# Kernel tuning notes

Hardware: AMD Instinct MI355X
Metric: run time of the kernel (lower is better)

The kernel has to match this reference:

```python
import jax, jax.numpy as jnp
import numpy as np

DIM, NH, NS = 384, 8, 3
HID = int(DIM * 4.0)
R1 = max(1, int(min(DIM, HID) * 0.5))   # 192
R2 = max(1, int(min(HID, DIM) * 0.5))   # 192
SPLIT = DIM // NS                        # 128
HD = DIM // NH                           # 48


def _ln(x, g, b, eps=1e-6):
    m = jnp.mean(x, axis=-1, keepdims=True)
    v = jnp.mean(jnp.square(x - m), axis=-1, keepdims=True)
    return (x - m) * jax.lax.rsqrt(v + eps) * g + b


def _dwconv(x, w, b):
    # x: [B, SPLIT, H, W]; w: [SPLIT, 1, 3, 3] depthwise (groups=SPLIT)
    y = jax.lax.conv_general_dilated(
        x, w, window_strides=(1, 1), padding='SAME',
        dimension_numbers=('NCHW', 'OIHW', 'NCHW'),
        feature_group_count=SPLIT)
    return y + b[None, :, None, None]


def setup_inputs() -> dict:
    key = jax.random.key(0)
    ks = jax.random.split(key, 16)
    s = lambda *sh: 0.02
    inp = {
        'x': jax.random.normal(ks[0], (16, DIM, 56, 56), jnp.float32),
        'dw_w0': jax.random.normal(ks[1], (SPLIT, 1, 3, 3), jnp.float32) * 0.1,
        'dw_b0': jnp.zeros((SPLIT,), jnp.float32),
        'dw_w1': jax.random.normal(ks[2], (SPLIT, 1, 3, 3), jnp.float32) * 0.1,
        'dw_b1': jnp.zeros((SPLIT,), jnp.float32),
        'ln1_g': jnp.ones((DIM,), jnp.float32),
        'ln1_b': jnp.zeros((DIM,), jnp.float32),
        'qkv_w': jax.random.normal(ks[3], (DIM, 3 * DIM), jnp.float32) * 0.02,
        'proj_w': jax.random.normal(ks[4], (DIM, DIM), jnp.float32) * 0.02,
        'proj_b': jnp.zeros((DIM,), jnp.float32),
        'ln2_g': jnp.ones((DIM,), jnp.float32),
        'ln2_b': jnp.zeros((DIM,), jnp.float32),
        'mlp1_dw': jax.random.normal(ks[5], (DIM, R1), jnp.float32) * 0.02,
        'mlp1_uw': jax.random.normal(ks[6], (R1, HID), jnp.float32) * 0.02,
        'mlp1_ub': jnp.zeros((HID,), jnp.float32),
        'mlp2_dw': jax.random.normal(ks[7], (HID, R2), jnp.float32) * 0.02,
        'mlp2_uw': jax.random.normal(ks[8], (R2, DIM), jnp.float32) * 0.02,
        'mlp2_ub': jnp.zeros((DIM,), jnp.float32),
    }
    return inp


def reference(x, dw_w0, dw_b0, dw_w1, dw_b1, ln1_g, ln1_b, qkv_w,
              proj_w, proj_b, ln2_g, ln2_b,
              mlp1_dw, mlp1_uw, mlp1_ub, mlp2_dw, mlp2_uw, mlp2_ub):
    B, C, H, W = x.shape
    # multi-scale depthwise residual chain
    s0, s1, s2 = jnp.split(x, NS, axis=1)
    s1 = _dwconv(s1 + s0, dw_w0, dw_b0)
    s2 = _dwconv(s2 + s1, dw_w1, dw_b1)
    x = jnp.concatenate([s0, s1, s2], axis=1)

    N = H * W
    x_flat = jnp.transpose(x.reshape(B, C, N), (0, 2, 1))  # [B, N, C]
    y = _ln(x_flat, ln1_g, ln1_b)
    qkv = (y @ qkv_w).reshape(B, N, 3, NH, HD)
    q = jnp.transpose(qkv[:, :, 0], (0, 2, 3, 1))  # [B, NH, HD, N]
    k = jnp.transpose(qkv[:, :, 1], (0, 2, 3, 1))
    v = jnp.transpose(qkv[:, :, 2], (0, 2, 3, 1))
    # L2 normalize over token dim (XCA)
    q = q / jnp.maximum(jnp.linalg.norm(q, axis=-1, keepdims=True), 1e-12)
    k = k / jnp.maximum(jnp.linalg.norm(k, axis=-1, keepdims=True), 1e-12)
    attn = jnp.einsum('bhdn,bhen->bhde', q, k)  # [B, NH, HD, HD]
    attn = jax.nn.softmax(attn, axis=-1)
    y = jnp.einsum('bhde,bhen->bhdn', attn, v)  # [B, NH, HD, N]
    y = jnp.transpose(y, (0, 3, 1, 2)).reshape(B, N, C)
    y = y @ proj_w + proj_b
    x_flat = x_flat + y

    z = _ln(x_flat, ln2_g, ln2_b)
    h = jax.nn.gelu((z @ mlp1_dw) @ mlp1_uw + mlp1_ub, approximate=False)
    z = (h @ mlp2_dw) @ mlp2_uw + mlp2_ub
    x_flat = x_flat + z
    return jnp.transpose(x_flat, (0, 2, 1)).reshape(B, C, H, W)
```

## Files before the change

### kernel.cpp

```cpp
#include <hip/hip_runtime.h>


typedef __attribute__((ext_vector_type(8))) short short8;
typedef __attribute__((ext_vector_type(4))) float floatx4;

#define NB 16
#define DIM 384
#define NTOK 3136
#define TTOK 50176
#define NH 8
#define HD 48

__device__ __forceinline__ unsigned short f2bf(float f) {
  union { float f; unsigned int u; } v; v.f = f;
  unsigned int u = v.u;
  unsigned int r = (u + 0x7FFFu + ((u >> 16) & 1u)) >> 16;
  return (unsigned short)r;
}
__device__ __forceinline__ float bf2f(unsigned short h) {
  union { unsigned int u; float f; } v; v.u = ((unsigned int)h) << 16;
  return v.f;
}

__device__ __forceinline__ void gload_lds16(const unsigned short* g, unsigned short* l) {
  __builtin_amdgcn_global_load_lds(
      (const __attribute__((address_space(1))) unsigned int*)g,
      (__attribute__((address_space(3))) unsigned int*)l, 16, 0, 0);
}

__global__ void wtrans(const float* __restrict__ w, unsigned short* __restrict__ wt,
                       int K, int N) {
  int g = blockIdx.x * 256 + threadIdx.x;
  if (g < K * N) {
    int k = g / N, n = g % N;
    wt[(size_t)n * K + k] = f2bf(w[g]);
  }
}

__global__ void dwconv(const float* __restrict__ a, long bsA,
                       const float* __restrict__ b2, long bsB,
                       const float* __restrict__ w, const float* __restrict__ bias,
                       float* __restrict__ dst) {
  int g = blockIdx.x * 256 + threadIdx.x;
  int xx = g % 56;
  int yy = (g / 56) % 56;
  int c  = (g / NTOK) % 128;
  int b  = g / (NTOK * 128);
  const float* pa = a  + (size_t)b * bsA + (size_t)c * NTOK;
  const float* pb = b2 + (size_t)b * bsB + (size_t)c * NTOK;
  float acc = bias[c];
  #pragma unroll
  for (int ky = 0; ky < 3; ky++) {
    int y2 = yy + ky - 1;
    if (y2 < 0 || y2 >= 56) continue;
    #pragma unroll
    for (int kx = 0; kx < 3; kx++) {
      int x2 = xx + kx - 1;
      if (x2 < 0 || x2 >= 56) continue;
      acc += w[c * 9 + ky * 3 + kx] * (pa[y2 * 56 + x2] + pb[y2 * 56 + x2]);
    }
  }
  dst[((size_t)b * 128 + c) * NTOK + yy * 56 + xx] = acc;
}

__global__ __launch_bounds__(256) void build_ln1(
    const float* __restrict__ x, const float* __restrict__ s1,
    const float* __restrict__ s2, const float* __restrict__ g,
    const float* __restrict__ bb, float* __restrict__ xflat,
    unsigned short* __restrict__ y) {
  __shared__ float tile[384 * 33];
  __shared__ float psum[8][32], psumsq[8][32];
  __shared__ float smean[32], srs[32];
  int blk = blockIdx.x;
  int b = blk / 98, n0 = (blk % 98) * 32;
  int t = threadIdx.x;
  int nl = t & 31, crow = t >> 5;

  #pragma unroll 4
  for (int i = 0; i < 48; i++) {
    int c = i * 8 + crow;
    float v;
    if (c < 128)      v = x[((size_t)b * DIM + c) * NTOK + n0 + nl];
    else if (c < 256) v = s1[((size_t)b * 128 + (c - 128)) * NTOK + n0 + nl];
    else              v = s2[((size_t)b * 128 + (c - 256)) * NTOK + n0 + nl];
    tile[c * 33 + nl] = v;
  }
  __syncthreads();

  {
    int seg = t >> 5, tok = t & 31;
    float s = 0.f, sq = 0.f;
    #pragma unroll 8
    for (int cc = 0; cc < 48; cc++) {
      float v = tile[(seg * 48 + cc) * 33 + tok];
      s += v; sq += v * v;
    }
    psum[seg][tok] = s; psumsq[seg][tok] = sq;
  }
  __syncthreads();
  if (t < 32) {
    float s = 0.f, sq = 0.f;
    #pragma unroll
    for (int seg = 0; seg < 8; seg++) { s += psum[seg][t]; sq += psumsq[seg][t]; }
    float mean = s * (1.f / DIM);
    float var = sq * (1.f / DIM) - mean * mean;
    smean[t] = mean;
    srs[t] = rsqrtf(var + 1e-6f);
  }
  __syncthreads();

  #pragma unroll 4
  for (int i = 0; i < 48; i++) {
    int idx = i * 256 + t;
    int tok = idx / 384, c = idx - tok * 384;
    float v = tile[c * 33 + tok];
    size_t o = (size_t)(b * NTOK + n0 + tok) * DIM + c;
    xflat[o] = v;
    y[o] = f2bf((v - smean[tok]) * srs[tok] * g[c] + bb[c]);
  }
}

__global__ __launch_bounds__(256) void ln_rows(
    const float* __restrict__ in, const float* __restrict__ g,
    const float* __restrict__ bb, unsigned short* __restrict__ out) {
  int tkn = blockIdx.x * 4 + (threadIdx.x >> 6);
  int lane = threadIdx.x & 63;
  const float* row = in + (size_t)tkn * DIM;
  float v[6];
  float s = 0.f, sq = 0.f;
  #pragma unroll
  for (int i = 0; i < 6; i++) {
    int c = lane + i * 64;
    v[i] = row[c]; s += v[i]; sq += v[i] * v[i];
  }
  #pragma unroll
  for (int off = 32; off; off >>= 1) {
    s += __shfl_xor(s, off);
    sq += __shfl_xor(sq, off);
  }
  float mean = s * (1.f / DIM);
  float var = sq * (1.f / DIM) - mean * mean;
  float rs = rsqrtf(var + 1e-6f);
  #pragma unroll
  for (int i = 0; i < 6; i++) {
    int c = lane + i * 64;
    out[(size_t)tkn * DIM + c] = f2bf((v[i] - mean) * rs * g[c] + bb[c]);
  }
}

template<int BN, int MODE>
__global__ __launch_bounds__(256) void gemm128(
    const unsigned short* __restrict__ A, const unsigned short* __restrict__ Bt,
    const float* __restrict__ bias, const float* __restrict__ resid,
    void* __restrict__ out, int M, int N, int K) {
  constexpr int MT = (BN == 128) ? 4 : 2;
  constexpr int NT = 4;
  __shared__ __align__(16) unsigned short As[128 * 32];
  __shared__ __align__(16) unsigned short Bs[BN * 32];
  const int tid = threadIdx.x;
  const int w = tid >> 6, lane = tid & 63;
  const int quad = lane >> 4, r16 = lane & 15;
  const int row0 = blockIdx.y * 128, col0 = blockIdx.x * BN;
  const int wm = (BN == 128) ? (w >> 1) * 64 : w * 32;
  const int wn = (BN == 128) ? (w & 1) * 64 : 0;
  const int lrow = lane >> 2;
  const int lcol = (lane & 3) * 8;

  const unsigned short* aP0 = A + (size_t)(row0 + w * 32 + lrow) * K + lcol;
  const unsigned short* aP1 = aP0 + (size_t)16 * K;
  const unsigned short* bP0 = Bt + (size_t)(col0 + ((BN == 128) ? w * 32 : w * 16) + lrow) * K + lcol;
  const unsigned short* bP1 = bP0 + (size_t)16 * K;

  floatx4 acc[MT][NT] = {};

  for (int k0 = 0; k0 < K; k0 += 32) {
    gload_lds16(aP0 + k0, &As[(2 * w) * 512]);
    gload_lds16(aP1 + k0, &As[(2 * w + 1) * 512]);
    if (BN == 128) {
      gload_lds16(bP0 + k0, &Bs[(2 * w) * 512]);
      gload_lds16(bP1 + k0, &Bs[(2 * w + 1) * 512]);
    } else {
      gload_lds16(bP0 + k0, &Bs[w * 512]);
    }
    __syncthreads();
    short8 af[MT], bfr[NT];
    #pragma unroll
    for (int mi = 0; mi < MT; mi++)
      af[mi] = *(const short8*)(&As[(wm + mi * 16 + r16) * 32 + quad * 8]);
    #pragma unroll
    for (int ni = 0; ni < NT; ni++)
      bfr[ni] = *(const short8*)(&Bs[(wn + ni * 16 + r16) * 32 + quad * 8]);
    #pragma unroll
    for (int mi = 0; mi < MT; mi++)
      #pragma unroll
      for (int ni = 0; ni < NT; ni++)
        acc[mi][ni] = __builtin_amdgcn_mfma_f32_16x16x32_bf16(af[mi], bfr[ni], acc[mi][ni], 0, 0, 0);
    __syncthreads();
  }

  #pragma unroll
  for (int mi = 0; mi < MT; mi++)
    #pragma unroll
    for (int ni = 0; ni < NT; ni++)
      #pragma unroll
      for (int p = 0; p < 4; p++) {
        int row = row0 + wm + mi * 16 + quad * 4 + p;
        int col = col0 + wn + ni * 16 + r16;
        size_t idx = (size_t)row * N + col;
        float v = acc[mi][ni][p];
        if (MODE == 0) {
          ((unsigned short*)out)[idx] = f2bf(v);
        } else if (MODE == 1) {
          v += bias[col];
          v = 0.5f * v * (1.0f + erff(v * 0.70710678118654752f));
          ((unsigned short*)out)[idx] = f2bf(v);
        } else {
          v += bias[col] + resid[idx];
          ((float*)out)[idx] = v;
        }
      }
}

__global__ __launch_bounds__(256) void attn_partial(
    const unsigned short* __restrict__ qkv, float* __restrict__ S_part,
    float* __restrict__ sq_part) {
  __shared__ float qs[48 * 68];
  __shared__ float ks[48 * 68];
  int blk = blockIdx.x;
  int b = blk / 56, rem = blk % 56;
  int h = rem / 7, chunk = rem % 7;
  int t = threadIdx.x;
  int d0 = (t >> 4) * 3, e0 = (t & 15) * 3;

  floatx4 acc4[3][3] = {};
  floatx4 sqq4 = {}, sqk4 = {};

  for (int tile = 0; tile < 7; tile++) {
    __syncthreads();
    int tb = chunk * 448 + tile * 64;
    #pragma unroll
    for (int i = 0; i < 12; i++) {
      int idx = t + i * 256;
      int r = idx / 48, d = idx - r * 48;
      size_t ro = ((size_t)b * NTOK + tb + r) * 1152 + h * HD;
      qs[d * 68 + r] = bf2f(qkv[ro + d]);
      ks[d * 68 + r] = bf2f(qkv[ro + 384 + d]);
    }
    __syncthreads();
    #pragma unroll 4
    for (int r4 = 0; r4 < 16; r4++) {
      floatx4 q4[3], k4[3];
      #pragma unroll
      for (int j = 0; j < 3; j++) {
        q4[j] = *(const floatx4*)(&qs[(d0 + j) * 68 + r4 * 4]);
        k4[j] = *(const floatx4*)(&ks[(e0 + j) * 68 + r4 * 4]);
      }
      #pragma unroll
      for (int i = 0; i < 3; i++)
        #pragma unroll
        for (int j = 0; j < 3; j++)
          acc4[i][j] += q4[i] * k4[j];
    }
    if (t < 48) {
      #pragma unroll 4
      for (int r4 = 0; r4 < 16; r4++) {
        floatx4 v = *(const floatx4*)(&qs[t * 68 + r4 * 4]);
        sqq4 += v * v;
      }
    } else if (t >= 64 && t < 112) {
      int e = t - 64;
      #pragma unroll 4
      for (int r4 = 0; r4 < 16; r4++) {
        floatx4 v = *(const floatx4*)(&ks[e * 68 + r4 * 4]);
        sqk4 += v * v;
      }
    }
  }

  int bh = b * NH + h;
  float* Sp = S_part + ((size_t)chunk * 128 + bh) * 2304;
  #pragma unroll
  for (int i = 0; i < 3; i++)
    #pragma unroll
    for (int j = 0; j < 3; j++)
      Sp[(d0 + i) * 48 + e0 + j] = acc4[i][j][0] + acc4[i][j][1] + acc4[i][j][2] + acc4[i][j][3];
  if (t < 48)
    sq_part[(size_t)chunk * 12288 + b * 768 + h * HD + t] = sqq4[0] + sqq4[1] + sqq4[2] + sqq4[3];
  else if (t >= 64 && t < 112)
    sq_part[(size_t)chunk * 12288 + b * 768 + 384 + h * HD + (t - 64)] = sqk4[0] + sqk4[1] + sqk4[2] + sqk4[3];
}

__global__ __launch_bounds__(256) void attn_finish(
    const float* __restrict__ S_part, const float* __restrict__ sq_part,
    float* __restrict__ attnb) {
  __shared__ float qn[48], kn[48];
  __shared__ float Ss[48 * 49];
  int bh = blockIdx.x, b = bh >> 3, h = bh & 7;
  int t = threadIdx.x;
  if (t < 48) {
    float s = 0.f;
    #pragma unroll
    for (int p = 0; p < 7; p++) s += sq_part[(size_t)p * 12288 + b * 768 + h * HD + t];
    qn[t] = fmaxf(sqrtf(s), 1e-12f);
  } else if (t >= 64 && t < 112) {
    int e = t - 64;
    float s = 0.f;
    #pragma unroll
    for (int p = 0; p < 7; p++) s += sq_part[(size_t)p * 12288 + b * 768 + 384 + h * HD + e];
    kn[e] = fmaxf(sqrtf(s), 1e-12f);
  }
  __syncthreads();
  #pragma unroll
  for (int j = 0; j < 9; j++) {
    int idx = j * 256 + t;
    float s = 0.f;
    #pragma unroll
    for (int p = 0; p < 7; p++) s += S_part[((size_t)p * 128 + bh) * 2304 + idx];
    int d = idx / 48, e = idx - d * 48;
    Ss[d * 49 + e] = s / (qn[d] * kn[e]);
  }
  __syncthreads();
  if (t < 48) {
    float m = -1e30f;
    for (int e = 0; e < 48; e++) m = fmaxf(m, Ss[t * 49 + e]);
    float ssum = 0.f;
    float ex[48];
    for (int e = 0; e < 48; e++) { ex[e] = expf(Ss[t * 49 + e] - m); ssum += ex[e]; }
    float inv = 1.f / ssum;
    float* op = attnb + (size_t)bh * 2304 + t * 48;
    for (int e = 0; e < 48; e++) op[e] = ex[e] * inv;
  }
}

__global__ __launch_bounds__(256) void attn_apply(
    const unsigned short* __restrict__ qkv, const float* __restrict__ attnb,
    unsigned short* __restrict__ yat) {
  __shared__ float at[48 * 52];
  __shared__ float vs[64 * 56];
  int bh = blockIdx.x / 49, chunk = blockIdx.x % 49;
  int b = bh >> 3, h = bh & 7;
  int t = threadIdx.x;
  int lane = t & 63, w = t >> 6;
  #pragma unroll
  for (int i = 0; i < 9; i++) {
    int idx = t + i * 256;
    if (idx < 2304) at[(idx / 48) * 52 + idx % 48] = attnb[(size_t)bh * 2304 + idx];
  }
  #pragma unroll
  for (int i = 0; i < 12; i++) {
    int idx = t + i * 256;
    int r = idx / 48, d = idx - r * 48;
    vs[r * 56 + d] = bf2f(qkv[((size_t)b * NTOK + chunk * 64 + r) * 1152 + 768 + h * HD + d]);
  }
  __syncthreads();
  floatx4 v4[12];
  #pragma unroll
  for (int j = 0; j < 12; j++)
    v4[j] = *(const floatx4*)(&vs[lane * 56 + j * 4]);
  float r[12];
  #pragma unroll
  for (int dd = 0; dd < 12; dd++) {
    int d = w * 12 + dd;
    floatx4 a = {};
    #pragma unroll
    for (int j = 0; j < 12; j++)
      a += *(const floatx4*)(&at[d * 52 + j * 4]) * v4[j];
    r[dd] = a[0] + a[1] + a[2] + a[3];
  }
  size_t wo = ((size_t)b * NTOK + chunk * 64 + lane) * DIM + h * HD + w * 12;
  unsigned int* op = (unsigned int*)(yat + wo);
  #pragma unroll
  for (int j = 0; j < 6; j++)
    op[j] = (unsigned int)f2bf(r[2 * j]) | ((unsigned int)f2bf(r[2 * j + 1]) << 16);
}

__global__ __launch_bounds__(256) void transpose_out(const float* __restrict__ in,
                                                     float* __restrict__ out) {
  __shared__ float tile[32][33];
  int b = blockIdx.z, ct = blockIdx.y, nt = blockIdx.x;
  int t = threadIdx.x;
  int cc = t & 31, rr = t >> 5;
  #pragma unroll
  for (int i = 0; i < 4; i++) {
    int nn = rr + i * 8;
    tile[nn][cc] = in[((size_t)b * NTOK + nt * 32 + nn) * DIM + ct * 32 + cc];
  }
  __syncthreads();
  #pragma unroll
  for (int i = 0; i < 4; i++) {
    int c2 = rr + i * 8;
    out[((size_t)b * DIM + ct * 32 + c2) * NTOK + nt * 32 + cc] = tile[cc][c2];
  }
}

extern "C" void kernel_launch(void* const* d_in, const int* in_sizes, int n_in,
                              void* d_out, int out_size, void* d_ws, size_t ws_size,
                              hipStream_t stream) {
  const float* x       = (const float*)d_in[0];
  const float* dw_w0   = (const float*)d_in[1];
  const float* dw_b0   = (const float*)d_in[2];
  const float* dw_w1   = (const float*)d_in[3];
  const float* dw_b1   = (const float*)d_in[4];
  const float* ln1_g   = (const float*)d_in[5];
  const float* ln1_b   = (const float*)d_in[6];
  const float* qkv_w   = (const float*)d_in[7];
  const float* proj_w  = (const float*)d_in[8];
  const float* proj_b  = (const float*)d_in[9];
  const float* ln2_g   = (const float*)d_in[10];
  const float* ln2_b   = (const float*)d_in[11];
  const float* mlp1_dw = (const float*)d_in[12];
  const float* mlp1_uw = (const float*)d_in[13];
  const float* mlp1_ub = (const float*)d_in[14];
  const float* mlp2_dw = (const float*)d_in[15];
  const float* mlp2_uw = (const float*)d_in[16];
  const float* mlp2_ub = (const float*)d_in[17];
  float* out = (float*)d_out;
  char* ws = (char*)d_ws;

  float*          xflat = (float*)(ws + 0);
  unsigned short* qkvb  = (unsigned short*)(ws + 77070336);
  float*          s1ws  = (float*)(ws + 77070336);
  float*          s2ws  = (float*)(ws + 102760448);
  unsigned short* ybf   = (unsigned short*)(ws + 192675840);
  float*          S_part  = (float*)(ws + 192675840);
  float*          sq_part = (float*)(ws + 200933376);
  unsigned short* yat   = (unsigned short*)(ws + 192675840);
  float*          xres  = (float*)(ws + 77070336);
  unsigned short* zbf   = (unsigned short*)(ws + 0);
  unsigned short* h1    = (unsigned short*)(ws + 38535168);
  unsigned short* h3    = (unsigned short*)(ws + 57802752);
  unsigned short* h2    = (unsigned short*)(ws + 154140672);
  unsigned short* qkvT  = (unsigned short*)(ws + 231211008);
  unsigned short* projT = (unsigned short*)(ws + 232095744);
  unsigned short* m1dT  = (unsigned short*)(ws + 232390656);
  unsigned short* m1uT  = (unsigned short*)(ws + 232538112);
  unsigned short* m2dT  = (unsigned short*)(ws + 233127936);
  unsigned short* m2uT  = (unsigned short*)(ws + 233717760);
  float*          attnb = (float*)(ws + 233914368);

  wtrans<<<1728, 256, 0, stream>>>(qkv_w, qkvT, 384, 1152);
  wtrans<<<576, 256, 0, stream>>>(proj_w, projT, 384, 384);
  wtrans<<<288, 256, 0, stream>>>(mlp1_dw, m1dT, 384, 192);
  wtrans<<<1152, 256, 0, stream>>>(mlp1_uw, m1uT, 192, 1536);
  wtrans<<<1152, 256, 0, stream>>>(mlp2_dw, m2dT, 1536, 192);
  wtrans<<<288, 256, 0, stream>>>(mlp2_uw, m2uT, 192, 384);

  dwconv<<<25088, 256, 0, stream>>>(x + 128 * NTOK, (long)DIM * NTOK,
                                    x, (long)DIM * NTOK, dw_w0, dw_b0, s1ws);
  dwconv<<<25088, 256, 0, stream>>>(x + 256 * NTOK, (long)DIM * NTOK,
                                    s1ws, (long)128 * NTOK, dw_w1, dw_b1, s2ws);

  build_ln1<<<1568, 256, 0, stream>>>(x, s1ws, s2ws, ln1_g, ln1_b, xflat, ybf);

  gemm128<128, 0><<<dim3(9, 392), 256, 0, stream>>>(ybf, qkvT, nullptr, nullptr,
                                                    qkvb, TTOK, 1152, 384);
  attn_partial<<<NB * NH * 7, 256, 0, stream>>>(qkvb, S_part, sq_part);
  attn_finish<<<NB * NH, 256, 0, stream>>>(S_part, sq_part, attnb);
  attn_apply<<<NB * NH * 49, 256, 0, stream>>>(qkvb, attnb, yat);

  gemm128<128, 2><<<dim3(3, 392), 256, 0, stream>>>(yat, projT, proj_b, xflat,
                                                    xres, TTOK, 384, 384);
  ln_rows<<<12544, 256, 0, stream>>>(xres, ln2_g, ln2_b, zbf);
  gemm128<64, 0><<<dim3(3, 392), 256, 0, stream>>>(zbf, m1dT, nullptr, nullptr,
                                                   h1, TTOK, 192, 384);
  for (int half = 0; half < 2; half++) {
    const unsigned short* h1p = h1 + (size_t)half * 25088 * 192;
    unsigned short* h3p = h3 + (size_t)half * 25088 * 192;
    gemm128<128, 1><<<dim3(12, 196), 256, 0, stream>>>(h1p, m1uT, mlp1_ub, nullptr,
                                                       h2, 25088, 1536, 192);
    gemm128<64, 0><<<dim3(3, 196), 256, 0, stream>>>(h2, m2dT, nullptr, nullptr,
                                                     h3p, 25088, 192, 1536);
  }
  gemm128<128, 2><<<dim3(3, 392), 256, 0, stream>>>(h3, m2uT, mlp2_ub, xres,
                                                    xres, TTOK, 384, 192);
  transpose_out<<<dim3(98, 12, 16), 256, 0, stream>>>(xres, out);
}
```

Baseline: 888.3 us.

## Compute XCA scores via per-batch Gram matrix of LN1 output instead of Q/K

```diff
diff --git a/kernel.cpp b/kernel.cpp
--- a/kernel.cpp
+++ b/kernel.cpp
@@ -67,7 +67,7 @@
     const float* __restrict__ x, const float* __restrict__ s1,
     const float* __restrict__ s2, const float* __restrict__ g,
     const float* __restrict__ bb, float* __restrict__ xflat,
-    unsigned short* __restrict__ y) {
+    unsigned short* __restrict__ y, unsigned short* __restrict__ yT) {
   __shared__ float tile[384 * 33];
   __shared__ float psum[8][32], psumsq[8][32];
   __shared__ float smean[32], srs[32];
@@ -114,9 +114,18 @@
     int idx = i * 256 + t;
     int tok = idx / 384, c = idx - tok * 384;
     float v = tile[c * 33 + tok];
+    float vn = (v - smean[tok]) * srs[tok] * g[c] + bb[c];
     size_t o = (size_t)(b * NTOK + n0 + tok) * DIM + c;
     xflat[o] = v;
-    y[o] = f2bf((v - smean[tok]) * srs[tok] * g[c] + bb[c]);
+    y[o] = f2bf(vn);
+    tile[c * 33 + tok] = vn;
+  }
+  __syncthreads();
+  #pragma unroll 4
+  for (int i = 0; i < 48; i++) {
+    int idx = i * 256 + t;
+    int c = idx >> 5, tok = idx & 31;
+    yT[((size_t)b * DIM + c) * NTOK + n0 + tok] = f2bf(tile[c * 33 + tok]);
   }
 }
 
@@ -149,10 +158,11 @@
 }
 
 template<int BN, int MODE>
-__global__ __launch_bounds__(256) void gemm128(
+__global__ __launch_bounds__(256) void gemmx(
     const unsigned short* __restrict__ A, const unsigned short* __restrict__ Bt,
     const float* __restrict__ bias, const float* __restrict__ resid,
-    void* __restrict__ out, int M, int N, int K) {
+    void* __restrict__ out, int M, int N, int K, int lda, int ldb,
+    int nsplit, long aBatch, long aSplit, long bBatch, long bSplit, long cBatch) {
   constexpr int MT = (BN == 128) ? 4 : 2;
   constexpr int NT = 4;
   __shared__ __align__(16) unsigned short As[128 * 32];
@@ -160,16 +170,30 @@
   const int tid = threadIdx.x;
   const int w = tid >> 6, lane = tid & 63;
   const int quad = lane >> 4, r16 = lane & 15;
-  const int row0 = blockIdx.y * 128, col0 = blockIdx.x * BN;
+
+  const int nwg = gridDim.x * gridDim.y;
+  const int bid = blockIdx.y * gridDim.x + blockIdx.x;
+  const int q8 = nwg >> 3, r8 = nwg & 7;
+  const int xcd = bid & 7, loc = bid >> 3;
+  const int swz = (xcd < r8 ? xcd * (q8 + 1) : r8 * (q8 + 1) + (xcd - r8) * q8) + loc;
+  const int bx = swz % gridDim.x, by = swz / gridDim.x;
+  const int row0 = by * 128, col0 = bx * BN;
+
+  const int z = blockIdx.z;
+  const int bz = z / nsplit, sz = z - bz * nsplit;
+  A  += bz * aBatch + sz * aSplit;
+  Bt += bz * bBatch + sz * bSplit;
+  const size_t cOff = (size_t)z * cBatch;
+
   const int wm = (BN == 128) ? (w >> 1) * 64 : w * 32;
   const int wn = (BN == 128) ? (w & 1) * 64 : 0;
   const int lrow = lane >> 2;
   const int lcol = (lane & 3) * 8;
 
-  const unsigned short* aP0 = A + (size_t)(row0 + w * 32 + lrow) * K + lcol;
-  const unsigned short* aP1 = aP0 + (size_t)16 * K;
-  const unsigned short* bP0 = Bt + (size_t)(col0 + ((BN == 128) ? w * 32 : w * 16) + lrow) * K + lcol;
-  const unsigned short* bP1 = bP0 + (size_t)16 * K;
+  const unsigned short* aP0 = A + (size_t)(row0 + w * 32 + lrow) * lda + lcol;
+  const unsigned short* aP1 = aP0 + (size_t)16 * lda;
+  const unsigned short* bP0 = Bt + (size_t)(col0 + ((BN == 128) ? w * 32 : w * 16) + lrow) * ldb + lcol;
+  const unsigned short* bP1 = bP0 + (size_t)16 * ldb;
 
   floatx4 acc[MT][NT] = {};
 
@@ -209,117 +233,96 @@
         size_t idx = (size_t)row * N + col;
         float v = acc[mi][ni][p];
         if (MODE == 0) {
-          ((unsigned short*)out)[idx] = f2bf(v);
+          ((unsigned short*)out)[cOff + idx] = f2bf(v);
         } else if (MODE == 1) {
           v += bias[col];
           v = 0.5f * v * (1.0f + erff(v * 0.70710678118654752f));
           ((unsigned short*)out)[idx] = f2bf(v);
-        } else {
+        } else if (MODE == 2) {
           v += bias[col] + resid[idx];
           ((float*)out)[idx] = v;
+        } else {
+          ((float*)out)[cOff + idx] = v;
         }
       }
 }
 
-__global__ __launch_bounds__(256) void attn_partial(
-    const unsigned short* __restrict__ qkv, float* __restrict__ S_part,
-    float* __restrict__ sq_part) {
-  __shared__ float qs[48 * 68];
-  __shared__ float ks[48 * 68];
-  int blk = blockIdx.x;
-  int b = blk / 56, rem = blk % 56;
-  int h = rem / 7, chunk = rem % 7;
+__global__ __launch_bounds__(256) void gsum(const unsigned short* __restrict__ Gp,
+                                            unsigned short* __restrict__ Gbf) {
+  int b = blockIdx.x / 576;
+  int i = (blockIdx.x % 576) * 256 + threadIdx.x;
+  float s = 0.f;
+  #pragma unroll
+  for (int p = 0; p < 7; p++)
+    s += bf2f(Gp[((size_t)(b * 7 + p)) * 147456 + i]);
+  Gbf[(size_t)b * 147456 + i] = f2bf(s);
+}
+
+__global__ __launch_bounds__(256) void attn_finish2(
+    const float* __restrict__ P, const unsigned short* __restrict__ qkvT,
+    const float* __restrict__ qkv_w, float* __restrict__ attnb) {
+  __shared__ unsigned short wkT[48 * 392];
+  __shared__ float Ss[48 * 49];
+  __shared__ float qn[48], kn[48];
+  int bh = blockIdx.x, b = bh >> 3, h = bh & 7;
   int t = threadIdx.x;
+  const float* Pb = P + (size_t)b * 294912;
+
+  #pragma unroll
+  for (int i = 0; i < 9; i++) {
+    int idx = t + i * 256;
+    int e = idx / 48, j = idx - e * 48;
+    *(short8*)(&wkT[e * 392 + j * 8]) =
+        *(const short8*)(&qkvT[(size_t)(384 + h * 48 + e) * 384 + j * 8]);
+  }
+  if (t < 48) {
+    const float* pr = Pb + (size_t)(h * 48 + t) * 384;
+    const float* wc = qkv_w + h * 48 + t;
+    float s = 0.f;
+    #pragma unroll 8
+    for (int c = 0; c < 384; c++) s += pr[c] * wc[(size_t)c * 1152];
+    qn[t] = fmaxf(sqrtf(fmaxf(s, 0.f)), 1e-12f);
+  } else if (t >= 64 && t < 112) {
+    int e = t - 64;
+    const float* pr = Pb + (size_t)(384 + h * 48 + e) * 384;
+    const float* wc = qkv_w + 384 + h * 48 + e;
+    float s = 0.f;
+    #pragma unroll 8
+    for (int c = 0; c < 384; c++) s += pr[c] * wc[(size_t)c * 1152];
+    kn[e] = fmaxf(sqrtf(fmaxf(s, 0.f)), 1e-12f);
+  }
+  __syncthreads();
+
   int d0 = (t >> 4) * 3, e0 = (t & 15) * 3;
-
-  floatx4 acc4[3][3] = {};
-  floatx4 sqq4 = {}, sqk4 = {};
-
-  for (int tile = 0; tile < 7; tile++) {
-    __syncthreads();
-    int tb = chunk * 448 + tile * 64;
-    #pragma unroll
-    for (int i = 0; i < 12; i++) {
-      int idx = t + i * 256;
-      int r = idx / 48, d = idx - r * 48;
-      size_t ro = ((size_t)b * NTOK + tb + r) * 1152 + h * HD;
-      qs[d * 68 + r] = bf2f(qkv[ro + d]);
-      ks[d * 68 + r] = bf2f(qkv[ro + 384 + d]);
+  float acc[3][3] = {};
+  const float* pq0 = Pb + (size_t)(h * 48 + d0) * 384;
+  for (int c8 = 0; c8 < 48; c8++) {
+    floatx4 pv[3][2];
+    #pragma unroll
+    for (int i = 0; i < 3; i++) {
+      pv[i][0] = *(const floatx4*)(pq0 + (size_t)i * 384 + c8 * 8);
+      pv[i][1] = *(const floatx4*)(pq0 + (size_t)i * 384 + c8 * 8 + 4);
     }
-    __syncthreads();
-    #pragma unroll 4
-    for (int r4 = 0; r4 < 16; r4++) {
-      floatx4 q4[3], k4[3];
+    #pragma unroll
+    for (int j = 0; j < 3; j++) {
+      short8 wv = *(const short8*)(&wkT[(e0 + j) * 392 + c8 * 8]);
       #pragma unroll
-      for (int j = 0; j < 3; j++) {
-        q4[j] = *(const floatx4*)(&qs[(d0 + j) * 68 + r4 * 4]);
-        k4[j] = *(const floatx4*)(&ks[(e0 + j) * 68 + r4 * 4]);
-      }
-      #pragma unroll
-      for (int i = 0; i < 3; i++)
+      for (int kk = 0; kk < 4; kk++) {
+        float wa = bf2f((unsigned short)wv[kk]);
+        float wb = bf2f((unsigned short)wv[4 + kk]);
         #pragma unroll
-        for (int j = 0; j < 3; j++)
-          acc4[i][j] += q4[i] * k4[j];
-    }
-    if (t < 48) {
-      #pragma unroll 4
-      for (int r4 = 0; r4 < 16; r4++) {
-        floatx4 v = *(const floatx4*)(&qs[t * 68 + r4 * 4]);
-        sqq4 += v * v;
-      }
-    } else if (t >= 64 && t < 112) {
-      int e = t - 64;
-      #pragma unroll 4
-      for (int r4 = 0; r4 < 16; r4++) {
-        floatx4 v = *(const floatx4*)(&ks[e * 68 + r4 * 4]);
-        sqk4 += v * v;
+        for (int i = 0; i < 3; i++)
+          acc[i][j] += pv[i][0][kk] * wa + pv[i][1][kk] * wb;
       }
     }
   }
-
-  int bh = b * NH + h;
-  float* Sp = S_part + ((size_t)chunk * 128 + bh) * 2304;
   #pragma unroll
   for (int i = 0; i < 3; i++)
     #pragma unroll
     for (int j = 0; j < 3; j++)
-      Sp[(d0 + i) * 48 + e0 + j] = acc4[i][j][0] + acc4[i][j][1] + acc4[i][j][2] + acc4[i][j][3];
-  if (t < 48)
-    sq_part[(size_t)chunk * 12288 + b * 768 + h * HD + t] = sqq4[0] + sqq4[1] + sqq4[2] + sqq4[3];
-  else if (t >= 64 && t < 112)
-    sq_part[(size_t)chunk * 12288 + b * 768 + 384 + h * HD + (t - 64)] = sqk4[0] + sqk4[1] + sqk4[2] + sqk4[3];
-}
-
-__global__ __launch_bounds__(256) void attn_finish(
-    const float* __restrict__ S_part, const float* __restrict__ sq_part,
-    float* __restrict__ attnb) {
-  __shared__ float qn[48], kn[48];
-  __shared__ float Ss[48 * 49];
-  int bh = blockIdx.x, b = bh >> 3, h = bh & 7;
-  int t = threadIdx.x;
-  if (t < 48) {
-    float s = 0.f;
-    #pragma unroll
-    for (int p = 0; p < 7; p++) s += sq_part[(size_t)p * 12288 + b * 768 + h * HD + t];
-    qn[t] = fmaxf(sqrtf(s), 1e-12f);
-  } else if (t >= 64 && t < 112) {
-    int e = t - 64;
-    float s = 0.f;
-    #pragma unroll
-    for (int p = 0; p < 7; p++) s += sq_part[(size_t)p * 12288 + b * 768 + 384 + h * HD + e];
-    kn[e] = fmaxf(sqrtf(s), 1e-12f);
-  }
-  __syncthreads();
-  #pragma unroll
-  for (int j = 0; j < 9; j++) {
-    int idx = j * 256 + t;
-    float s = 0.f;
-    #pragma unroll
-    for (int p = 0; p < 7; p++) s += S_part[((size_t)p * 128 + bh) * 2304 + idx];
-    int d = idx / 48, e = idx - d * 48;
-    Ss[d * 49 + e] = s / (qn[d] * kn[e]);
-  }
-  __syncthreads();
+      Ss[(d0 + i) * 49 + e0 + j] = acc[i][j] / (qn[d0 + i] * kn[e0 + j]);
+  __syncthreads();
+
   if (t < 48) {
     float m = -1e30f;
     for (int e = 0; e < 48; e++) m = fmaxf(m, Ss[t * 49 + e]);
@@ -333,7 +336,7 @@
 }
 
 __global__ __launch_bounds__(256) void attn_apply(
-    const unsigned short* __restrict__ qkv, const float* __restrict__ attnb,
+    const unsigned short* __restrict__ vbf, const float* __restrict__ attnb,
     unsigned short* __restrict__ yat) {
   __shared__ float at[48 * 52];
   __shared__ float vs[64 * 56];
@@ -347,10 +350,21 @@
     if (idx < 2304) at[(idx / 48) * 52 + idx % 48] = attnb[(size_t)bh * 2304 + idx];
   }
   #pragma unroll
-  for (int i = 0; i < 12; i++) {
+  for (int i = 0; i < 2; i++) {
     int idx = t + i * 256;
-    int r = idx / 48, d = idx - r * 48;
-    vs[r * 56 + d] = bf2f(qkv[((size_t)b * NTOK + chunk * 64 + r) * 1152 + 768 + h * HD + d]);
+    if (idx < 384) {
+      int r = idx / 6, j = idx - r * 6;
+      short8 vv = *(const short8*)(&vbf[((size_t)b * NTOK + chunk * 64 + r) * 384
+                                        + h * HD + j * 8]);
+      floatx4 f0, f1;
+      #pragma unroll
+      for (int kk = 0; kk < 4; kk++) {
+        f0[kk] = bf2f((unsigned short)vv[kk]);
+        f1[kk] = bf2f((unsigned short)vv[4 + kk]);
+      }
+      *(floatx4*)(&vs[r * 56 + j * 8]) = f0;
+      *(floatx4*)(&vs[r * 56 + j * 8 + 4]) = f1;
+    }
   }
   __syncthreads();
   floatx4 v4[12];
@@ -418,13 +432,15 @@
   char* ws = (char*)d_ws;
 
   float*          xflat = (float*)(ws + 0);
-  unsigned short* qkvb  = (unsigned short*)(ws + 77070336);
   float*          s1ws  = (float*)(ws + 77070336);
   float*          s2ws  = (float*)(ws + 102760448);
-  unsigned short* ybf   = (unsigned short*)(ws + 192675840);
-  float*          S_part  = (float*)(ws + 192675840);
-  float*          sq_part = (float*)(ws + 200933376);
-  unsigned short* yat   = (unsigned short*)(ws + 192675840);
+  unsigned short* vbf   = (unsigned short*)(ws + 77070336);
+  unsigned short* ybf   = (unsigned short*)(ws + 128450560);
+  unsigned short* ybfT  = (unsigned short*)(ws + 166985728);
+  unsigned short* G_part= (unsigned short*)(ws + 128450560);
+  unsigned short* Gbf   = (unsigned short*)(ws + 205520896);
+  float*          P     = (float*)(ws + 210239488);
+  unsigned short* yat   = (unsigned short*)(ws + 166985728);
   float*          xres  = (float*)(ws + 77070336);
   unsigned short* zbf   = (unsigned short*)(ws + 0);
   unsigned short* h1    = (unsigned short*)(ws + 38535168);
@@ -450,28 +466,45 @@
   dwconv<<<25088, 256, 0, stream>>>(x + 256 * NTOK, (long)DIM * NTOK,
                                     s1ws, (long)128 * NTOK, dw_w1, dw_b1, s2ws);
 
-  build_ln1<<<1568, 256, 0, stream>>>(x, s1ws, s2ws, ln1_g, ln1_b, xflat, ybf);
-
-  gemm128<128, 0><<<dim3(9, 392), 256, 0, stream>>>(ybf, qkvT, nullptr, nullptr,
-                                                    qkvb, TTOK, 1152, 384);
-  attn_partial<<<NB * NH * 7, 256, 0, stream>>>(qkvb, S_part, sq_part);
-  attn_finish<<<NB * NH, 256, 0, stream>>>(S_part, sq_part, attnb);
-  attn_apply<<<NB * NH * 49, 256, 0, stream>>>(qkvb, attnb, yat);
-
-  gemm128<128, 2><<<dim3(3, 392), 256, 0, stream>>>(yat, projT, proj_b, xflat,
-                                                    xres, TTOK, 384, 384);
+  build_ln1<<<1568, 256, 0, stream>>>(x, s1ws, s2ws, ln1_g, ln1_b, xflat, ybf, ybfT);
+
+  gemmx<128, 0><<<dim3(3, 392), 256, 0, stream>>>(
+      ybf, qkvT + 768 * 384, nullptr, nullptr, vbf,
+      TTOK, 384, 384, 384, 384, 1, 0, 0, 0, 0, 0);
+
+  gemmx<128, 0><<<dim3(3, 3, 112), 256, 0, stream>>>(
+      ybfT, ybfT, nullptr, nullptr, G_part,
+      384, 384, 448, 3136, 3136, 7,
+      (long)384 * 3136, 448L, (long)384 * 3136, 448L, 147456L);
+  gsum<<<9216, 256, 0, stream>>>(G_part, Gbf);
+
+  gemmx<128, 3><<<dim3(3, 6, 16), 256, 0, stream>>>(
+      qkvT, Gbf, nullptr, nullptr, P,
+      768, 384, 384, 384, 384, 1,
+      0, 0, 147456L, 0, 294912L);
+  attn_finish2<<<NB * NH, 256, 0, stream>>>(P, qkvT, qkv_w, attnb);
+
+  attn_apply<<<NB * NH * 49, 256, 0, stream>>>(vbf, attnb, yat);
+
+  gemmx<128, 2><<<dim3(3, 392), 256, 0, stream>>>(
+      yat, projT, proj_b, xflat, xres,
+      TTOK, 384, 384, 384, 384, 1, 0, 0, 0, 0, 0);
   ln_rows<<<12544, 256, 0, stream>>>(xres, ln2_g, ln2_b, zbf);
-  gemm128<64, 0><<<dim3(3, 392), 256, 0, stream>>>(zbf, m1dT, nullptr, nullptr,
-                                                   h1, TTOK, 192, 384);
+  gemmx<64, 0><<<dim3(3, 392), 256, 0, stream>>>(
+      zbf, m1dT, nullptr, nullptr, h1,
+      TTOK, 192, 384, 384, 384, 1, 0, 0, 0, 0, 0);
   for (int half = 0; half < 2; half++) {
     const unsigned short* h1p = h1 + (size_t)half * 25088 * 192;
     unsigned short* h3p = h3 + (size_t)half * 25088 * 192;
-    gemm128<128, 1><<<dim3(12, 196), 256, 0, stream>>>(h1p, m1uT, mlp1_ub, nullptr,
-                                                       h2, 25088, 1536, 192);
-    gemm128<64, 0><<<dim3(3, 196), 256, 0, stream>>>(h2, m2dT, nullptr, nullptr,
-                                                     h3p, 25088, 192, 1536);
-  }
-  gemm128<128, 2><<<dim3(3, 392), 256, 0, stream>>>(h3, m2uT, mlp2_ub, xres,
-                                                    xres, TTOK, 384, 192);
+    gemmx<128, 1><<<dim3(12, 196), 256, 0, stream>>>(
+        h1p, m1uT, mlp1_ub, nullptr, h2,
+        25088, 1536, 192, 192, 192, 1, 0, 0, 0, 0, 0);
+    gemmx<64, 0><<<dim3(3, 196), 256, 0, stream>>>(
+        h2, m2dT, nullptr, nullptr, h3p,
+        25088, 192, 1536, 1536, 1536, 1, 0, 0, 0, 0, 0);
+  }
+  gemmx<128, 2><<<dim3(3, 392), 256, 0, stream>>>(
+      h3, m2uT, mlp2_ub, xres, xres,
+      TTOK, 384, 192, 192, 192, 1, 0, 0, 0, 0, 0);
   transpose_out<<<dim3(98, 12, 16), 256, 0, stream>>>(xres, out);
 }
```

Result: faster. 816.9 us (median of 2 runs) (-8.0%).
